# Kernel optimization log

Measured on AMD Instinct MI355X. Metric: run time of the kernel, lower is better.

Reference implementation:

```python
import jax, jax.numpy as jnp
import numpy as np

N_NODES = 50000
N_EDGES = 800000
IN_DIM = 256
HEADS = 4
HEAD_DIM = 64  # out_dim // heads
NEG_SLOPE = 0.2  # PyG GATConv default


def setup_inputs() -> dict:
    key = jax.random.key(0)
    k1, k2, k3, k4, k5 = jax.random.split(key, 5)
    x = jax.random.normal(k1, (N_NODES, IN_DIM), dtype=jnp.float32)
    edge_index = jax.random.randint(k2, (2, N_EDGES), 0, N_NODES, dtype=jnp.int64)
    # Glorot-ish scaling
    W = jax.random.normal(k3, (IN_DIM, HEADS * HEAD_DIM), dtype=jnp.float32) * (1.0 / np.sqrt(IN_DIM))
    att_src = jax.random.normal(k4, (HEADS, HEAD_DIM), dtype=jnp.float32) * (1.0 / np.sqrt(HEAD_DIM))
    att_dst = jax.random.normal(k5, (HEADS, HEAD_DIM), dtype=jnp.float32) * (1.0 / np.sqrt(HEAD_DIM))
    bias = jnp.zeros((HEADS * HEAD_DIM,), dtype=jnp.float32)
    return {"x": x, "edge_index": edge_index, "W": W, "att_src": att_src,
            "att_dst": att_dst, "bias": bias}


def reference(x, edge_index, W, att_src, att_dst, bias):
    N = x.shape[0]
    # add self-loops (PyG GATConv default)
    loops = jnp.arange(N, dtype=edge_index.dtype)
    src = jnp.concatenate([edge_index[0], loops])
    dst = jnp.concatenate([edge_index[1], loops])

    h = (x @ W).reshape(N, HEADS, HEAD_DIM)          # [N,H,D]
    a_src = jnp.einsum('nhd,hd->nh', h, att_src)     # [N,H]
    a_dst = jnp.einsum('nhd,hd->nh', h, att_dst)     # [N,H]

    e = a_src[src] + a_dst[dst]                      # [E,H]
    e = jax.nn.leaky_relu(e, NEG_SLOPE)

    # segment softmax over edges sharing a destination node
    m = jax.ops.segment_max(e, dst, num_segments=N)  # [N,H]
    e = jnp.exp(e - m[dst])
    denom = jax.ops.segment_sum(e, dst, num_segments=N)  # [N,H]
    alpha = e / denom[dst]                           # [E,H]

    msg = alpha[:, :, None] * h[src]                 # [E,H,D]
    out = jax.ops.segment_sum(msg, dst, num_segments=N)  # [N,H,D]
    return out.reshape(N, HEADS * HEAD_DIM) + bias
```

## Files before the change

### kernel.cpp

```cpp
#include <hip/hip_runtime.h>
#include <hip/hip_bf16.h>

#define N_NODES 50000
#define N_EDGES 800000
#define IN_DIM 256
#define HEADS 4
#define HEAD_DIM 64
#define OUT_DIM 256
#define NEG_SLOPE 0.2f
#define M_PAD 50048
#define SEG_CAP 64

#define GEMM_BLOCKS 782
#define SCAT_BLOCKS 3125
#define MEGA_BLOCKS (GEMM_BLOCKS + SCAT_BLOCKS)
#define PREP_BLOCKS 260
#define AGG_BLOCKS 50000

typedef float floatx4 __attribute__((ext_vector_type(4)));
typedef short shortx8 __attribute__((ext_vector_type(8)));

__global__ __launch_bounds__(256) void prep(const float* __restrict__ W,
                                            ushort* __restrict__ Wt,
                                            int* __restrict__ cnt,
                                            int* __restrict__ csr) {
    int b = blockIdx.x;
    if (b < 64) {
        int t = b * 256 + threadIdx.x;
        int n = t >> 6;
        int k = (t & 63) << 2;
        ushort4 o;
        o.x = __bfloat16_as_ushort(__float2bfloat16(W[(size_t)(k + 0) * OUT_DIM + n]));
        o.y = __bfloat16_as_ushort(__float2bfloat16(W[(size_t)(k + 1) * OUT_DIM + n]));
        o.z = __bfloat16_as_ushort(__float2bfloat16(W[(size_t)(k + 2) * OUT_DIM + n]));
        o.w = __bfloat16_as_ushort(__float2bfloat16(W[(size_t)(k + 3) * OUT_DIM + n]));
        *(ushort4*)&Wt[(size_t)n * IN_DIM + k] = o;
    } else {
        int t = (b - 64) * 256 + threadIdx.x;
        if (t < N_NODES) csr[t << 6] = t;
        if (t < 12500) ((int4*)cnt)[t] = make_int4(1, 1, 1, 1);
    }
}

__global__ __launch_bounds__(256) void mega_kernel(const float* __restrict__ x,
                                                   const ushort* __restrict__ Wt,
                                                   const float* __restrict__ att_src,
                                                   const float* __restrict__ att_dst,
                                                   const int* __restrict__ e_src,
                                                   const int* __restrict__ e_dst,
                                                   int* __restrict__ cnt,
                                                   int* __restrict__ csr,
                                                   ushort* __restrict__ h2,
                                                   float* __restrict__ asrc,
                                                   float* __restrict__ adst) {
    __shared__ float A_lds[2][64 * 32];

    if (blockIdx.x >= GEMM_BLOCKS) {
        int id = (blockIdx.x - GEMM_BLOCKS) * 256 + threadIdx.x;
        if (id < N_EDGES) {
            int s = e_src[id];
            int d = e_dst[id];
            int pos = atomicAdd(&cnt[d], 1);
            if (pos < SEG_CAP) csr[(d << 6) + pos] = s;
        }
        return;
    }

    const int tid = threadIdx.x;
    const int w = tid >> 6;
    const int lane = tid & 63;
    const int quad = lane >> 4;
    const int l16 = lane & 15;
    const int row0 = blockIdx.x * 64;

    auto stage = [&](int buf, int k0) {
#pragma unroll
        for (int i = 0; i < 2; ++i) {
            int s = i * 256 + tid;
            int row = s >> 3;
            int cg = (s & 7) ^ (row & 7);
            int gr = row0 + row;
            if (gr > N_NODES - 1) gr = N_NODES - 1;
            const float* src = &x[(size_t)gr * IN_DIM + k0 + cg * 4];
            __builtin_amdgcn_global_load_lds(
                (const __attribute__((address_space(1))) unsigned int*)src,
                (__attribute__((address_space(3))) unsigned int*)&A_lds[buf][s * 4],
                16, 0, 0);
        }
    };

    floatx4 acc[4][4] = {};
    const ushort* wtb = Wt + (size_t)(w * 64 + l16) * IN_DIM + quad * 8;

    stage(0, 0);
    __syncthreads();
#pragma unroll 2
    for (int t = 0; t < 8; ++t) {
        int cur = t & 1;
        if (t < 7) stage(cur ^ 1, (t + 1) * 32);
        int k0 = t * 32;
        shortx8 bfr[4], af[4];
#pragma unroll
        for (int c = 0; c < 4; ++c)
            bfr[c] = *(const shortx8*)(wtb + (size_t)c * 16 * IN_DIM + k0);
#pragma unroll
        for (int r = 0; r < 4; ++r) {
            const int row = r * 16 + l16;
            const int sw = row & 7;
            const float* Ab = &A_lds[cur][row * 32];
            float4 f0 = *(const float4*)&Ab[((2 * quad) ^ sw) * 4];
            float4 f1 = *(const float4*)&Ab[((2 * quad + 1) ^ sw) * 4];
            float f[8] = {f0.x, f0.y, f0.z, f0.w, f1.x, f1.y, f1.z, f1.w};
            alignas(16) ushort a8[8];
#pragma unroll
            for (int u = 0; u < 8; ++u)
                a8[u] = __bfloat16_as_ushort(__float2bfloat16(f[u]));
            af[r] = *(const shortx8*)a8;
        }
#pragma unroll
        for (int r = 0; r < 4; ++r)
#pragma unroll
            for (int c = 0; c < 4; ++c)
                acc[r][c] = __builtin_amdgcn_mfma_f32_16x16x32_bf16(bfr[c], af[r],
                                                                    acc[r][c], 0, 0, 0);
        __syncthreads();
    }

    float as_cj[16], ad_cj[16];
#pragma unroll
    for (int c = 0; c < 4; ++c)
#pragma unroll
        for (int j = 0; j < 4; ++j) {
            int col = w * 64 + c * 16 + quad * 4 + j;
            as_cj[c * 4 + j] = att_src[col];
            ad_cj[c * 4 + j] = att_dst[col];
        }
#pragma unroll
    for (int r = 0; r < 4; ++r) {
        float s = 0.f, d = 0.f;
        alignas(16) ushort o16[16];
#pragma unroll
        for (int c = 0; c < 4; ++c)
#pragma unroll
            for (int j = 0; j < 4; ++j) {
                float v = acc[r][c][j];
                s = fmaf(v, as_cj[c * 4 + j], s);
                d = fmaf(v, ad_cj[c * 4 + j], d);
                o16[c * 4 + j] = __bfloat16_as_ushort(__float2bfloat16(v));
            }
        s += __shfl_xor(s, 16);
        s += __shfl_xor(s, 32);
        d += __shfl_xor(d, 16);
        d += __shfl_xor(d, 32);
        int gr = row0 + r * 16 + l16;
        if (quad == 0 && gr < N_NODES) {
            asrc[gr * HEADS + w] = s;
            adst[gr * HEADS + w] = d;
        }
        ushort* hp = h2 + (size_t)gr * OUT_DIM + w * 64 + quad * 16;
        *(uint4*)hp = *(const uint4*)&o16[0];
        *(uint4*)(hp + 8) = *(const uint4*)&o16[8];
    }
}

__global__ __launch_bounds__(256) void aggregate_v10(const uint2* __restrict__ h2,
                                                     const float* __restrict__ a_src,
                                                     const float* __restrict__ a_dst,
                                                     const int* __restrict__ cnt,
                                                     const int* __restrict__ csr,
                                                     const float* __restrict__ bias,
                                                     float* __restrict__ out) {
    int bid = blockIdx.x;
    int h = (bid & 7) >> 1;
    int nb = ((bid >> 3) << 1) | (bid & 1);
    int n = (nb << 2) + (threadIdx.x >> 6);
    int lane = threadIdx.x & 63;
    int eg = lane >> 4;
    int l = lane & 15;
    int col0 = (h << 6) + ((l & 3) << 4) + (((l >> 2) & 3) << 2);
    const uint2* h2h = h2 + (h << 4) + l;
    int beg = n << 6;
    int cn = min(cnt[n], SEG_CAP);
    float adv = a_dst[(n << 2) + h];

    float den = 0.f;
    float acc0 = 0.f, acc1 = 0.f, acc2 = 0.f, acc3 = 0.f;
    int nb8 = (cn + 7) >> 3;
    for (int b = 0; b < nb8; ++b) {
        int e0 = (b << 3) + (eg << 1);
        int2 s2 = *(const int2*)&csr[beg + e0];
        bool a0 = e0 < cn, a1 = e0 + 1 < cn;
        int s0 = a0 ? s2.x : 0;
        int s1 = a1 ? s2.y : 0;
        float as0 = a_src[(s0 << 2) + h];
        float as1 = a_src[(s1 << 2) + h];
        uint2 hv0 = h2h[(size_t)s0 * 64];
        uint2 hv1 = h2h[(size_t)s1 * 64];
        float ex0 = as0 + adv; ex0 = fmaxf(ex0, NEG_SLOPE * ex0);
        float ex1 = as1 + adv; ex1 = fmaxf(ex1, NEG_SLOPE * ex1);
        float p0 = a0 ? __expf(ex0) : 0.f;
        float p1 = a1 ? __expf(ex1) : 0.f;
        den += p0 + p1;
        acc0 = fmaf(p0, __uint_as_float(hv0.x << 16), acc0);
        acc1 = fmaf(p0, __uint_as_float(hv0.x & 0xffff0000u), acc1);
        acc2 = fmaf(p0, __uint_as_float(hv0.y << 16), acc2);
        acc3 = fmaf(p0, __uint_as_float(hv0.y & 0xffff0000u), acc3);
        acc0 = fmaf(p1, __uint_as_float(hv1.x << 16), acc0);
        acc1 = fmaf(p1, __uint_as_float(hv1.x & 0xffff0000u), acc1);
        acc2 = fmaf(p1, __uint_as_float(hv1.y << 16), acc2);
        acc3 = fmaf(p1, __uint_as_float(hv1.y & 0xffff0000u), acc3);
    }
    den  += __shfl_xor(den, 16);   den  += __shfl_xor(den, 32);
    acc0 += __shfl_xor(acc0, 16);  acc0 += __shfl_xor(acc0, 32);
    acc1 += __shfl_xor(acc1, 16);  acc1 += __shfl_xor(acc1, 32);
    acc2 += __shfl_xor(acc2, 16);  acc2 += __shfl_xor(acc2, 32);
    acc3 += __shfl_xor(acc3, 16);  acc3 += __shfl_xor(acc3, 32);

    if (eg == 0) {
        float idv = 1.0f / den;
        float4 bi = *(const float4*)&bias[col0];
        float4 o = make_float4(acc0 * idv + bi.x, acc1 * idv + bi.y,
                               acc2 * idv + bi.z, acc3 * idv + bi.w);
        *(float4*)&out[(size_t)n * OUT_DIM + col0] = o;
    }
}

extern "C" void kernel_launch(void* const* d_in, const int* in_sizes, int n_in,
                              void* d_out, int out_size, void* d_ws, size_t ws_size,
                              hipStream_t stream) {
    const float* x = (const float*)d_in[0];
    const int* ei = (const int*)d_in[1];
    const float* W = (const float*)d_in[2];
    const float* att_src = (const float*)d_in[3];
    const float* att_dst = (const float*)d_in[4];
    const float* bias = (const float*)d_in[5];
    float* out = (float*)d_out;

    const int* e_src = ei;
    const int* e_dst = ei + N_EDGES;

    char* p = (char*)d_ws;
    auto alloc = [&](size_t bytes) {
        void* r = (void*)p;
        p += (bytes + 255) & ~(size_t)255;
        return r;
    };
    ushort* h2   = (ushort*)alloc((size_t)M_PAD * OUT_DIM * 2);
    float* asrc  = (float*)alloc((size_t)N_NODES * HEADS * 4);
    float* adst  = (float*)alloc((size_t)N_NODES * HEADS * 4);
    int* cnt     = (int*)alloc((size_t)N_NODES * 4);
    int* csr     = (int*)alloc((size_t)N_NODES * SEG_CAP * 4);
    ushort* Wt   = (ushort*)alloc((size_t)IN_DIM * OUT_DIM * 2);

    prep<<<PREP_BLOCKS, 256, 0, stream>>>(W, Wt, cnt, csr);
    mega_kernel<<<MEGA_BLOCKS, 256, 0, stream>>>(x, Wt, att_src, att_dst, e_src, e_dst,
                                                 cnt, csr, h2, asrc, adst);
    aggregate_v10<<<AGG_BLOCKS, 256, 0, stream>>>((const uint2*)h2, asrc, adst,
                                                  cnt, csr, bias, out);
}
```

Baseline: 259.9 us.

## Aggregate all heads per wave with full-row gathers and exp2-prescaled scores

The aggregation kernel now assigns one wave per destination node covering all four heads, instead of one wave per node-head. Each lane computes one edge-head score, and the scores are broadcast by shuffle while 8 edges' full 512-byte h rows are gathered per iteration. This cuts redundant csr/a_src loads and gives each gather wider contiguous memory accesses. Attention logits are prescaled by log2(e) in the GEMM epilogue so the raw exp2 instruction can be used, and prep now zero-fills the whole csr array so padded entries index node 0 safely, which adds extra memset traffic.

```diff
diff --git a/kernel.cpp b/kernel.cpp
--- a/kernel.cpp
+++ b/kernel.cpp
@@ -8,14 +8,15 @@
 #define HEAD_DIM 64
 #define OUT_DIM 256
 #define NEG_SLOPE 0.2f
+#define LOG2E 1.44269504088896f
 #define M_PAD 50048
 #define SEG_CAP 64
 
 #define GEMM_BLOCKS 782
 #define SCAT_BLOCKS 3125
 #define MEGA_BLOCKS (GEMM_BLOCKS + SCAT_BLOCKS)
-#define PREP_BLOCKS 260
-#define AGG_BLOCKS 50000
+#define PREP_BLOCKS 3238
+#define AGG_BLOCKS 12500
 
 typedef float floatx4 __attribute__((ext_vector_type(4)));
 typedef short shortx8 __attribute__((ext_vector_type(8)));
@@ -35,9 +36,13 @@
         o.z = __bfloat16_as_ushort(__float2bfloat16(W[(size_t)(k + 2) * OUT_DIM + n]));
         o.w = __bfloat16_as_ushort(__float2bfloat16(W[(size_t)(k + 3) * OUT_DIM + n]));
         *(ushort4*)&Wt[(size_t)n * IN_DIM + k] = o;
+    } else if (b < 64 + 3125) {
+        int t = (b - 64) * 256 + threadIdx.x;
+        int4 v = make_int4(0, 0, 0, 0);
+        if ((t & 15) == 0) v.x = t >> 4;
+        ((int4*)csr)[t] = v;
     } else {
-        int t = (b - 64) * 256 + threadIdx.x;
-        if (t < N_NODES) csr[t << 6] = t;
+        int t = (b - 64 - 3125) * 256 + threadIdx.x;
         if (t < 12500) ((int4*)cnt)[t] = make_int4(1, 1, 1, 1);
     }
 }
@@ -154,8 +159,8 @@
         d += __shfl_xor(d, 32);
         int gr = row0 + r * 16 + l16;
         if (quad == 0 && gr < N_NODES) {
-            asrc[gr * HEADS + w] = s;
-            adst[gr * HEADS + w] = d;
+            asrc[gr * HEADS + w] = s * LOG2E;
+            adst[gr * HEADS + w] = d * LOG2E;
         }
         ushort* hp = h2 + (size_t)gr * OUT_DIM + w * 64 + quad * 16;
         *(uint4*)hp = *(const uint4*)&o16[0];
@@ -163,66 +168,64 @@
     }
 }
 
-__global__ __launch_bounds__(256) void aggregate_v10(const uint2* __restrict__ h2,
+__global__ __launch_bounds__(256) void aggregate_v11(const uint2* __restrict__ h2,
                                                      const float* __restrict__ a_src,
                                                      const float* __restrict__ a_dst,
                                                      const int* __restrict__ cnt,
                                                      const int* __restrict__ csr,
                                                      const float* __restrict__ bias,
                                                      float* __restrict__ out) {
-    int bid = blockIdx.x;
-    int h = (bid & 7) >> 1;
-    int nb = ((bid >> 3) << 1) | (bid & 1);
-    int n = (nb << 2) + (threadIdx.x >> 6);
+    int n = blockIdx.x * 4 + (threadIdx.x >> 6);
+    if (n >= N_NODES) return;
     int lane = threadIdx.x & 63;
-    int eg = lane >> 4;
-    int l = lane & 15;
-    int col0 = (h << 6) + ((l & 3) << 4) + (((l >> 2) & 3) << 2);
-    const uint2* h2h = h2 + (h << 4) + l;
+    int oh = lane >> 4;
+    int col0 = (oh << 6) + ((lane & 3) << 4) + (((lane >> 2) & 3) << 2);
     int beg = n << 6;
     int cn = min(cnt[n], SEG_CAP);
-    float adv = a_dst[(n << 2) + h];
-
-    float den = 0.f;
+    int nb8 = (cn + 7) >> 3;
+    int e_l = (lane >> 2) & 7;
+    int h_l = lane & 3;
+    float adv_p = a_dst[(n << 2) + h_l];
+
+    float den_p = 0.f;
     float acc0 = 0.f, acc1 = 0.f, acc2 = 0.f, acc3 = 0.f;
-    int nb8 = (cn + 7) >> 3;
     for (int b = 0; b < nb8; ++b) {
-        int e0 = (b << 3) + (eg << 1);
-        int2 s2 = *(const int2*)&csr[beg + e0];
-        bool a0 = e0 < cn, a1 = e0 + 1 < cn;
-        int s0 = a0 ? s2.x : 0;
-        int s1 = a1 ? s2.y : 0;
-        float as0 = a_src[(s0 << 2) + h];
-        float as1 = a_src[(s1 << 2) + h];
-        uint2 hv0 = h2h[(size_t)s0 * 64];
-        uint2 hv1 = h2h[(size_t)s1 * 64];
-        float ex0 = as0 + adv; ex0 = fmaxf(ex0, NEG_SLOPE * ex0);
-        float ex1 = as1 + adv; ex1 = fmaxf(ex1, NEG_SLOPE * ex1);
-        float p0 = a0 ? __expf(ex0) : 0.f;
-        float p1 = a1 ? __expf(ex1) : 0.f;
-        den += p0 + p1;
-        acc0 = fmaf(p0, __uint_as_float(hv0.x << 16), acc0);
-        acc1 = fmaf(p0, __uint_as_float(hv0.x & 0xffff0000u), acc1);
-        acc2 = fmaf(p0, __uint_as_float(hv0.y << 16), acc2);
-        acc3 = fmaf(p0, __uint_as_float(hv0.y & 0xffff0000u), acc3);
-        acc0 = fmaf(p1, __uint_as_float(hv1.x << 16), acc0);
-        acc1 = fmaf(p1, __uint_as_float(hv1.x & 0xffff0000u), acc1);
-        acc2 = fmaf(p1, __uint_as_float(hv1.y << 16), acc2);
-        acc3 = fmaf(p1, __uint_as_float(hv1.y & 0xffff0000u), acc3);
-    }
-    den  += __shfl_xor(den, 16);   den  += __shfl_xor(den, 32);
-    acc0 += __shfl_xor(acc0, 16);  acc0 += __shfl_xor(acc0, 32);
-    acc1 += __shfl_xor(acc1, 16);  acc1 += __shfl_xor(acc1, 32);
-    acc2 += __shfl_xor(acc2, 16);  acc2 += __shfl_xor(acc2, 32);
-    acc3 += __shfl_xor(acc3, 16);  acc3 += __shfl_xor(acc3, 32);
-
-    if (eg == 0) {
-        float idv = 1.0f / den;
-        float4 bi = *(const float4*)&bias[col0];
-        float4 o = make_float4(acc0 * idv + bi.x, acc1 * idv + bi.y,
-                               acc2 * idv + bi.z, acc3 * idv + bi.w);
-        *(float4*)&out[(size_t)n * OUT_DIM + col0] = o;
-    }
+        int i = beg + (b << 3);
+        int4 sa = *(const int4*)&csr[i];
+        int4 sb = *(const int4*)&csr[i + 4];
+        int ss[8] = {sa.x, sa.y, sa.z, sa.w, sb.x, sb.y, sb.z, sb.w};
+        int sl = csr[i + e_l];
+        float asv = a_src[(sl << 2) + h_l];
+        float t = asv + adv_p;
+        float lk = fmaxf(t, t * NEG_SLOPE);
+        float pl = ((b << 3) + e_l < cn) ? __builtin_amdgcn_exp2f(lk) : 0.f;
+        den_p += pl;
+        float vp[8];
+#pragma unroll
+        for (int e = 0; e < 8; ++e)
+            vp[e] = __shfl(pl, (e << 2) + oh);
+        uint2 hv[8];
+#pragma unroll
+        for (int u = 0; u < 8; ++u)
+            hv[u] = h2[(size_t)ss[u] * 64 + lane];
+#pragma unroll
+        for (int u = 0; u < 8; ++u) {
+            float p = vp[u];
+            acc0 = fmaf(p, __uint_as_float(hv[u].x << 16), acc0);
+            acc1 = fmaf(p, __uint_as_float(hv[u].x & 0xffff0000u), acc1);
+            acc2 = fmaf(p, __uint_as_float(hv[u].y << 16), acc2);
+            acc3 = fmaf(p, __uint_as_float(hv[u].y & 0xffff0000u), acc3);
+        }
+    }
+    den_p += __shfl_xor(den_p, 4);
+    den_p += __shfl_xor(den_p, 8);
+    den_p += __shfl_xor(den_p, 16);
+    float den = __shfl(den_p, oh);
+    float idv = 1.0f / den;
+    float4 bi = *(const float4*)&bias[col0];
+    float4 o = make_float4(acc0 * idv + bi.x, acc1 * idv + bi.y,
+                           acc2 * idv + bi.z, acc3 * idv + bi.w);
+    *(float4*)&out[(size_t)n * OUT_DIM + col0] = o;
 }
 
 extern "C" void kernel_launch(void* const* d_in, const int* in_sizes, int n_in,
@@ -255,6 +258,6 @@
     prep<<<PREP_BLOCKS, 256, 0, stream>>>(W, Wt, cnt, csr);
     mega_kernel<<<MEGA_BLOCKS, 256, 0, stream>>>(x, Wt, att_src, att_dst, e_src, e_dst,
                                                  cnt, csr, h2, asrc, adst);
-    aggregate_v10<<<AGG_BLOCKS, 256, 0, stream>>>((const uint2*)h2, asrc, adst,
+    aggregate_v11<<<AGG_BLOCKS, 256, 0, stream>>>((const uint2*)h2, asrc, adst,
                                                   cnt, csr, bias, out);
 }
```

New measurement: 225.8 us. 1.15x faster.
